# Performance work log

Hardware: AMD Instinct MI355X
Metric: run time of the kernel (lower is better)

Reference implementation:

```python
import jax, jax.numpy as jnp
import numpy as np

B, L, D = 2, 1024, 1024
H = 16
NL = 2
DFF = 4 * D
EPS = 1e-5
W_SCALE = 0.02


def rmsnorm(x, w):
    # x * rsqrt(mean(x^2, -1) + eps) * w   (computed in fp32 as in the torch code)
    xf = x.astype(jnp.float32)
    n = xf * jax.lax.rsqrt(jnp.mean(xf * xf, axis=-1, keepdims=True) + EPS)
    return n.astype(x.dtype) * w


def setup_inputs() -> dict:
    key = jax.random.key(0)
    ks = jax.random.split(key, 10)
    x = jax.random.normal(ks[0], (B, L, D), dtype=jnp.float32)
    # torch nn.Linear weight layout: [out_features, in_features]; y = x @ W.T + b
    qw = jax.random.normal(ks[1], (NL, D, D), dtype=jnp.float32) * W_SCALE
    kw = jax.random.normal(ks[2], (NL, D, D), dtype=jnp.float32) * W_SCALE
    vw = jax.random.normal(ks[3], (NL, D, D), dtype=jnp.float32) * W_SCALE
    ow = jax.random.normal(ks[4], (NL, D, D), dtype=jnp.float32) * W_SCALE
    pn_w = jnp.ones((NL, D), dtype=jnp.float32)
    ln_w = jnp.ones((NL, D), dtype=jnp.float32)
    fc_w = jax.random.normal(ks[5], (NL, DFF, D), dtype=jnp.float32) * W_SCALE
    fc2_w = jax.random.normal(ks[6], (NL, D, DFF), dtype=jnp.float32) * W_SCALE
    fc2_b = jnp.zeros((NL, D), dtype=jnp.float32)
    return {"x": x, "qw": qw, "kw": kw, "vw": vw, "ow": ow,
            "pn_w": pn_w, "ln_w": ln_w, "fc_w": fc_w, "fc2_w": fc2_w, "fc2_b": fc2_b}


def reference(x, qw, kw, vw, ow, pn_w, ln_w, fc_w, fc2_w, fc2_b):
    d = D // H
    for i in range(NL):
        # --- LinearAttention block (dropout=0 -> identity) ---
        h = rmsnorm(x, pn_w[i])                                   # [B,L,D]
        Q = (h @ qw[i].T).reshape(B, L, H, d)
        K = (h @ kw[i].T).reshape(B, L, H, d)
        V = (h @ vw[i].T).reshape(B, L, H, d)
        # outer-product state per position, cumulated over L (causal linear attn)
        W = jnp.einsum('blhd,blhe->blhde', K, V)                  # [B,L,H,d,d]
        W = jnp.cumsum(W, axis=1)
        a = jnp.einsum('blhd,blhde->blhe', Q, W).reshape(B, L, D)
        x = x + a @ ow[i].T
        # --- MLP block ---
        m = rmsnorm(x, ln_w[i])
        f = jax.nn.gelu(m @ fc_w[i].T, approximate=False)         # torch nn.GELU default = exact
        x = x + f @ fc2_w[i].T + fc2_b[i]
    return x
```

## Files before the change

kernel.cpp:

```cpp
#include <hip/hip_runtime.h>

#define BB 2
#define LL 1024
#define DD 1024
#define HH 16
#define HD 64
#define DFFN 4096
#define MM (BB*LL)
#define QS 3072

using u16 = unsigned short;
typedef __bf16 bf16x8 __attribute__((ext_vector_type(8)));
typedef float f32x4 __attribute__((ext_vector_type(4)));

__device__ __forceinline__ float b2f(u16 u) {
  union { unsigned int i; float f; } v; v.i = ((unsigned int)u) << 16; return v.f;
}
__device__ __forceinline__ u16 f2b(float f) {
  union { float f; unsigned int i; } v; v.f = f;
  unsigned int x = v.i;
  return (u16)((x + 0x7fffu + ((x >> 16) & 1u)) >> 16);
}
__device__ __forceinline__ float gelu_exact(float x) {
  return 0.5f * x * (1.0f + erff(x * 0.70710678118654752f));
}
__device__ __forceinline__ void gl2lds16(const void* g, void* l) {
  __builtin_amdgcn_global_load_lds((const __attribute__((address_space(1))) void*)g,
                                   (__attribute__((address_space(3))) void*)l, 16, 0, 0);
}

template<int N>
__device__ __forceinline__ void s_wait_vm() {
  if constexpr (N == 0)       asm volatile("s_waitcnt vmcnt(0) lgkmcnt(0)" ::: "memory");
  else if constexpr (N == 4)  asm volatile("s_waitcnt vmcnt(4) lgkmcnt(0)" ::: "memory");
  else if constexpr (N == 6)  asm volatile("s_waitcnt vmcnt(6) lgkmcnt(0)" ::: "memory");
  else if constexpr (N == 8)  asm volatile("s_waitcnt vmcnt(8) lgkmcnt(0)" ::: "memory");
  else if constexpr (N == 12) asm volatile("s_waitcnt vmcnt(12) lgkmcnt(0)" ::: "memory");
  __builtin_amdgcn_sched_barrier(0);
}

__device__ __forceinline__ void xcd_remap(int& bx, int& by, int& bz) {
  const int gx = gridDim.x, gy = gridDim.y;
  const int nb = gx * gy * gridDim.z;
  int b = blockIdx.x + gx * (blockIdx.y + gy * blockIdx.z);
  if ((nb & 127) == 0) {
    const int xcd = b & 7, seq = b >> 3;
    b = (((seq >> 4) << 3) + xcd) * 16 + (seq & 15);
  }
  bx = b % gx; const int rest = b / gx;
  by = rest % gy; bz = rest / gy;
}

__global__ __launch_bounds__(256) void castw_kernel(const float* __restrict__ in,
                                                    u16* __restrict__ out, int n8) {
  int i = blockIdx.x * 256 + threadIdx.x;
  if (i >= n8) return;
  const float4 a = reinterpret_cast<const float4*>(in)[2 * i];
  const float4 b = reinterpret_cast<const float4*>(in)[2 * i + 1];
  uint4 o;
  o.x = (unsigned)f2b(a.x) | ((unsigned)f2b(a.y) << 16);
  o.y = (unsigned)f2b(a.z) | ((unsigned)f2b(a.w) << 16);
  o.z = (unsigned)f2b(b.x) | ((unsigned)f2b(b.y) << 16);
  o.w = (unsigned)f2b(b.z) | ((unsigned)f2b(b.w) << 16);
  reinterpret_cast<uint4*>(out)[i] = o;
}
__global__ __launch_bounds__(256) void castw3_kernel(const float* __restrict__ s0,
                                                     const float* __restrict__ s1,
                                                     const float* __restrict__ s2,
                                                     u16* __restrict__ out, int n8) {
  int i = blockIdx.x * 256 + threadIdx.x;
  if (i >= n8) return;
  const float* in = (blockIdx.y == 0) ? s0 : (blockIdx.y == 1) ? s1 : s2;
  u16* dst = out + (size_t)blockIdx.y * n8 * 8;
  const float4 a = reinterpret_cast<const float4*>(in)[2 * i];
  const float4 b = reinterpret_cast<const float4*>(in)[2 * i + 1];
  uint4 o;
  o.x = (unsigned)f2b(a.x) | ((unsigned)f2b(a.y) << 16);
  o.y = (unsigned)f2b(a.z) | ((unsigned)f2b(a.w) << 16);
  o.z = (unsigned)f2b(b.x) | ((unsigned)f2b(b.y) << 16);
  o.w = (unsigned)f2b(b.z) | ((unsigned)f2b(b.w) << 16);
  reinterpret_cast<uint4*>(dst)[i] = o;
}

__global__ __launch_bounds__(256) void init_out_kernel(float* __restrict__ out,
                                                       const float* __restrict__ resid,
                                                       const float* __restrict__ bias) {
  const int i = blockIdx.x * 256 + threadIdx.x;
  float4 v = reinterpret_cast<const float4*>(resid)[i];
  if (bias != nullptr) {
    const float4 bv = *reinterpret_cast<const float4*>(bias + ((i * 4) & (DD - 1)));
    v.x += bv.x; v.y += bv.y; v.z += bv.z; v.w += bv.w;
  }
  reinterpret_cast<float4*>(out)[i] = v;
}

__global__ __launch_bounds__(256) void rmsnorm_kernel(const float* __restrict__ x,
                                                      const float* __restrict__ w,
                                                      u16* __restrict__ out) {
  const int row = blockIdx.x, t = threadIdx.x;
  const float4 v = reinterpret_cast<const float4*>(x + (size_t)row * DD)[t];
  float ss = v.x*v.x + v.y*v.y + v.z*v.z + v.w*v.w;
  #pragma unroll
  for (int o = 32; o > 0; o >>= 1) ss += __shfl_down(ss, o);
  __shared__ float red[4];
  if ((t & 63) == 0) red[t >> 6] = ss;
  __syncthreads();
  const float inv = rsqrtf((red[0] + red[1] + red[2] + red[3]) * (1.0f / DD) + 1e-5f);
  const float4 wv = reinterpret_cast<const float4*>(w)[t];
  ushort4 o;
  o.x = f2b(v.x * inv * wv.x);
  o.y = f2b(v.y * inv * wv.y);
  o.z = f2b(v.z * inv * wv.z);
  o.w = f2b(v.w * inv * wv.w);
  reinterpret_cast<ushort4*>(out + (size_t)row * DD)[t] = o;
}

template<int ROWS, int NT>
__device__ __forceinline__ void dma32(const u16* __restrict__ g, int r0, int K, int kt,
                                      int t, u16* lds) {
  #pragma unroll
  for (int i = 0; i < ROWS * 4 / NT; i++) {
    const int c = i * NT + t;
    gl2lds16(g + (size_t)(r0 + (c >> 2)) * K + kt + (c & 3) * 8, &lds[c * 8]);
  }
}
__device__ __forceinline__ void mfma_tile32(const u16* Asb, const u16* Bsb,
                                            int wm, int wn, int fr, int fq, f32x4 acc[4][4]) {
  bf16x8 af[4], bfv[4];
  #pragma unroll
  for (int i = 0; i < 4; i++)
    af[i] = *reinterpret_cast<const bf16x8*>(&Asb[(wm + i * 16 + fr) * 32 + fq * 8]);
  #pragma unroll
  for (int j = 0; j < 4; j++)
    bfv[j] = *reinterpret_cast<const bf16x8*>(&Bsb[(wn + j * 16 + fr) * 32 + fq * 8]);
  #pragma unroll
  for (int i = 0; i < 4; i++)
    #pragma unroll
    for (int j = 0; j < 4; j++)
      acc[i][j] = __builtin_amdgcn_mfma_f32_16x16x32_bf16(af[i], bfv[j], acc[i][j], 0, 0, 0);
}

template<int BM, int BN>
__device__ __forceinline__ void gemm_pipeline(const u16* __restrict__ A,
                                              const u16* __restrict__ Wb,
                                              int K, int k0, int nt, int m0, int n0,
                                              u16* As, u16* Bs, int t,
                                              int wm, int wn, int fr, int fq,
                                              f32x4 acc[4][4]) {
  constexpr int NT = (BM / 64) * (BN / 64) * 64;
  constexpr int L = (BM + BN) * 4 / NT;
  #pragma unroll
  for (int s = 0; s < 3; ++s) {
    dma32<BM, NT>(A, m0, K, k0 + s * 32, t, As + s * BM * 32);
    dma32<BN, NT>(Wb, n0, K, k0 + s * 32, t, Bs + s * BN * 32);
  }
  int pb = 0;
  for (int tt = 0; tt < nt; ++tt) {
    const int ahead = nt - 1 - tt;
    if (ahead >= 2)      s_wait_vm<2 * L>();
    else if (ahead == 1) s_wait_vm<L>();
    else                 s_wait_vm<0>();
    __builtin_amdgcn_s_barrier();
    __builtin_amdgcn_sched_barrier(0);
    if (tt + 3 < nt) {
      int p3 = pb + 3; if (p3 >= 4) p3 -= 4;
      dma32<BM, NT>(A, m0, K, k0 + (tt + 3) * 32, t, As + p3 * BM * 32);
      dma32<BN, NT>(Wb, n0, K, k0 + (tt + 3) * 32, t, Bs + p3 * BN * 32);
      __builtin_amdgcn_sched_barrier(0);
    }
    mfma_tile32(As + pb * BM * 32, Bs + pb * BN * 32, wm, wn, fr, fq, acc);
    pb = (pb + 1) & 3;
  }
}

template<int BM, int BN, int ACT>
__global__ __launch_bounds__((BM/64)*(BN/64)*64)
void mfma_gemm(const u16* __restrict__ A, const u16* __restrict__ Wb,
               u16* __restrict__ Cb, int N, int K) {
  constexpr int WCOLS = BN / 64;
  __shared__ u16 As[4 * BM * 32];
  __shared__ u16 Bs[4 * BN * 32];
  int bx, by, bz;
  xcd_remap(bx, by, bz);
  const int t = threadIdx.x;
  const int lane = t & 63, w = t >> 6;
  const int wm = (w / WCOLS) * 64, wn = (w % WCOLS) * 64;
  const int m0 = by * BM, n0 = bx * BN;
  const int fr = lane & 15, fq = lane >> 4;

  f32x4 acc[4][4] = {};
  gemm_pipeline<BM, BN>(A, Wb, K, 0, K / 32, m0, n0, As, Bs, t, wm, wn, fr, fq, acc);

  #pragma unroll
  for (int i = 0; i < 4; i++)
    #pragma unroll
    for (int j = 0; j < 4; j++)
      #pragma unroll
      for (int r = 0; r < 4; r++) {
        const int row = m0 + wm + i * 16 + fq * 4 + r;
        const int col = n0 + wn + j * 16 + fr;
        float val = acc[i][j][r];
        if (ACT == 1) val = gelu_exact(val);
        Cb[(size_t)row * N + col] = f2b(val);
      }
}

template<int BM, int BN, int SPLIT>
__global__ __launch_bounds__((BM/64)*(BN/64)*64)
void mfma_gemm_sk(const u16* __restrict__ A, const u16* __restrict__ Wb,
                  float* __restrict__ Co, int N, int K) {
  constexpr int WCOLS = BN / 64;
  __shared__ u16 As[4 * BM * 32];
  __shared__ u16 Bs[4 * BN * 32];
  int bx, by, bz;
  xcd_remap(bx, by, bz);
  const int t = threadIdx.x;
  const int lane = t & 63, w = t >> 6;
  const int wm = (w / WCOLS) * 64, wn = (w % WCOLS) * 64;
  const int m0 = by * BM, n0 = bx * BN;
  const int fr = lane & 15, fq = lane >> 4;
  const int Kc = K / SPLIT, k0 = bz * Kc;

  f32x4 acc[4][4] = {};
  gemm_pipeline<BM, BN>(A, Wb, K, k0, Kc / 32, m0, n0, As, Bs, t, wm, wn, fr, fq, acc);

  #pragma unroll
  for (int i = 0; i < 4; i++)
    #pragma unroll
    for (int j = 0; j < 4; j++)
      #pragma unroll
      for (int r = 0; r < 4; r++) {
        const int row = m0 + wm + i * 16 + fq * 4 + r;
        const int col = n0 + wn + j * 16 + fr;
        unsafeAtomicAdd(&Co[(size_t)row * N + col], acc[i][j][r]);
      }
}

__global__ __launch_bounds__(256) void kv_trans(const u16* __restrict__ QKV,
                                                u16* __restrict__ Kt, u16* __restrict__ Vt) {
  __shared__ u16 T[64][72];
  const int tile = blockIdx.x;
  const int h2 = blockIdx.y;
  const int b = blockIdx.z;
  const int h = h2 & 15, which = h2 >> 4;
  const int t = threadIdx.x;
  const int pos = t >> 2, d0 = (t & 3) * 16;
  const u16* src = QKV + ((size_t)(b * LL) + tile * 64 + pos) * QS + 1024 + which * 1024 + h * HD + d0;
  union { uint4 u[2]; u16 s[16]; } pk;
  pk.u[0] = reinterpret_cast<const uint4*>(src)[0];
  pk.u[1] = reinterpret_cast<const uint4*>(src)[1];
  #pragma unroll
  for (int j = 0; j < 16; j++) T[d0 + j][pos] = pk.s[j];
  __syncthreads();
  const int d = t >> 2, p0 = (t & 3) * 16;
  u16* dst = (which ? Vt : Kt) + ((size_t)(b * HH + h) * HD + d) * LL + tile * 64 + p0;
  union { uint4 u[2]; u16 s[16]; } ok;
  #pragma unroll
  for (int j = 0; j < 16; j++) ok.s[j] = T[d][p0 + j];
  reinterpret_cast<uint4*>(dst)[0] = ok.u[0];
  reinterpret_cast<uint4*>(dst)[1] = ok.u[1];
}

__global__ __launch_bounds__(256) void attn_phase1(const u16* __restrict__ QKV,
                                                   const u16* __restrict__ Kt,
                                                   const u16* __restrict__ Vt,
                                                   u16* __restrict__ Oa,
                                                   u16* __restrict__ Slt) {
  __shared__ u16 Ss[4][16][64];
  const int tile = blockIdx.x, h = blockIdx.y, b = blockIdx.z;
  const int t = threadIdx.x, lane = t & 63, w = t >> 6;
  const int fr = lane & 15, fq = lane >> 4;
  const size_t tok0 = (size_t)(b * LL + tile * 64);
  const size_t bh = (size_t)(b * HH + h);
  const u16* Qb  = QKV + tok0 * QS + h * HD;
  const u16* Kb  = Qb + 1024;
  const u16* Ktb = Kt + bh * (HD * LL) + tile * 64;
  const u16* Vtb = Vt + bh * (HD * LL) + tile * 64;

  bf16x8 aq[2], bk[4][2];
  #pragma unroll
  for (int kh = 0; kh < 2; kh++)
    aq[kh] = *reinterpret_cast<const bf16x8*>(Qb + (size_t)(16*w + fr) * QS + kh*32 + fq*8);
  #pragma unroll
  for (int n4 = 0; n4 < 4; n4++)
    #pragma unroll
    for (int kh = 0; kh < 2; kh++)
      bk[n4][kh] = *reinterpret_cast<const bf16x8*>(Kb + (size_t)(16*n4 + fr) * QS + kh*32 + fq*8);
  f32x4 sacc[4] = {};
  #pragma unroll
  for (int n4 = 0; n4 < 4; n4++) {
    sacc[n4] = __builtin_amdgcn_mfma_f32_16x16x32_bf16(aq[0], bk[n4][0], sacc[n4], 0, 0, 0);
    sacc[n4] = __builtin_amdgcn_mfma_f32_16x16x32_bf16(aq[1], bk[n4][1], sacc[n4], 0, 0, 0);
  }
  #pragma unroll
  for (int n4 = 0; n4 < 4; n4++)
    #pragma unroll
    for (int r = 0; r < 4; r++) {
      const bool keep = (16*w + 4*fq + r) >= (16*n4 + fr);
      Ss[w][4*fq + r][16*n4 + fr] = keep ? f2b(sacc[n4][r]) : (u16)0;
    }
  __syncthreads();

  bf16x8 va[2], kt[4][2];
  #pragma unroll
  for (int kh = 0; kh < 2; kh++)
    va[kh] = *reinterpret_cast<const bf16x8*>(Vtb + (size_t)(16*w + fr) * LL + kh*32 + fq*8);
  #pragma unroll
  for (int n4 = 0; n4 < 4; n4++)
    #pragma unroll
    for (int kh = 0; kh < 2; kh++)
      kt[n4][kh] = *reinterpret_cast<const bf16x8*>(Ktb + (size_t)(16*n4 + fr) * LL + kh*32 + fq*8);
  f32x4 lacc[4] = {};
  #pragma unroll
  for (int n4 = 0; n4 < 4; n4++) {
    lacc[n4] = __builtin_amdgcn_mfma_f32_16x16x32_bf16(va[0], kt[n4][0], lacc[n4], 0, 0, 0);
    lacc[n4] = __builtin_amdgcn_mfma_f32_16x16x32_bf16(va[1], kt[n4][1], lacc[n4], 0, 0, 0);
  }
  u16* So = Slt + (bh * 16 + tile) * 4096;
  #pragma unroll
  for (int n4 = 0; n4 < 4; n4++)
    #pragma unroll
    for (int r = 0; r < 4; r++)
      So[(size_t)(16*w + 4*fq + r) * 64 + 16*n4 + fr] = f2b(lacc[n4][r]);

  bf16x8 sa[2], vb[4][2];
  #pragma unroll
  for (int kh = 0; kh < 2; kh++)
    sa[kh] = *reinterpret_cast<const bf16x8*>(&Ss[w][fr][kh*32 + fq*8]);
  #pragma unroll
  for (int n4 = 0; n4 < 4; n4++)
    #pragma unroll
    for (int kh = 0; kh < 2; kh++)
      vb[n4][kh] = *reinterpret_cast<const bf16x8*>(Vtb + (size_t)(16*n4 + fr) * LL + kh*32 + fq*8);
  f32x4 oacc[4] = {};
  #pragma unroll
  for (int n4 = 0; n4 < 4; n4++) {
    oacc[n4] = __builtin_amdgcn_mfma_f32_16x16x32_bf16(sa[0], vb[n4][0], oacc[n4], 0, 0, 0);
    oacc[n4] = __builtin_amdgcn_mfma_f32_16x16x32_bf16(sa[1], vb[n4][1], oacc[n4], 0, 0, 0);
  }
  u16* Ob = Oa + (tok0 + 16*w) * DD + h * HD;
  #pragma unroll
  for (int n4 = 0; n4 < 4; n4++)
    #pragma unroll
    for (int r = 0; r < 4; r++)
      Ob[(size_t)(4*fq + r) * DD + 16*n4 + fr] = f2b(oacc[n4][r]);
}

__global__ __launch_bounds__(256) void attn_phase2(const u16* __restrict__ Slt,
                                                   u16* __restrict__ Wc) {
  const int rg = blockIdx.x, h = blockIdx.y, b = blockIdx.z;
  const size_t base = ((size_t)((b * HH + h) * 16)) * 4096 + rg * 512 + threadIdx.x * 2;
  float r0 = 0.f, r1 = 0.f;
  for (int tl = 0; tl < 16; tl++) {
    const size_t p = base + (size_t)tl * 4096;
    const unsigned d = *reinterpret_cast<const unsigned*>(Slt + p);
    *reinterpret_cast<unsigned*>(Wc + p) = (unsigned)f2b(r0) | ((unsigned)f2b(r1) << 16);
    r0 += b2f((u16)(d & 0xffff));
    r1 += b2f((u16)(d >> 16));
  }
}

__global__ __launch_bounds__(256) void attn_phase3(const u16* __restrict__ QKV,
                                                   const u16* __restrict__ Wc,
                                                   u16* __restrict__ Oa) {
  const int tile = blockIdx.x, h = blockIdx.y, b = blockIdx.z;
  const int t = threadIdx.x, lane = t & 63, w = t >> 6;
  const int fr = lane & 15, fq = lane >> 4;
  const size_t tok0 = (size_t)(b * LL + tile * 64);
  const size_t bh = (size_t)(b * HH + h);
  const u16* Qb = QKV + tok0 * QS + h * HD;
  const u16* Wb = Wc + (bh * 16 + tile) * 4096;

  bf16x8 aq[2], wb[4][2];
  #pragma unroll
  for (int kh = 0; kh < 2; kh++)
    aq[kh] = *reinterpret_cast<const bf16x8*>(Qb + (size_t)(16*w + fr) * QS + kh*32 + fq*8);
  #pragma unroll
  for (int n4 = 0; n4 < 4; n4++)
    #pragma unroll
    for (int kh = 0; kh < 2; kh++)
      wb[n4][kh] = *reinterpret_cast<const bf16x8*>(Wb + (size_t)(16*n4 + fr) * 64 + kh*32 + fq*8);
  f32x4 oacc[4] = {};
  #pragma unroll
  for (int n4 = 0; n4 < 4; n4++) {
    oacc[n4] = __builtin_amdgcn_mfma_f32_16x16x32_bf16(aq[0], wb[n4][0], oacc[n4], 0, 0, 0);
    oacc[n4] = __builtin_amdgcn_mfma_f32_16x16x32_bf16(aq[1], wb[n4][1], oacc[n4], 0, 0, 0);
  }
  u16* Ob = Oa + (tok0 + 16*w) * DD + h * HD;
  #pragma unroll
  for (int n4 = 0; n4 < 4; n4++)
    #pragma unroll
    for (int r = 0; r < 4; r++) {
      const size_t idx = (size_t)(4*fq + r) * DD + 16*n4 + fr;
      Ob[idx] = f2b(b2f(Ob[idx]) + oacc[n4][r]);
    }
}

extern "C" void kernel_launch(void* const* d_in, const int* in_sizes, int n_in,
                              void* d_out, int out_size, void* d_ws, size_t ws_size,
                              hipStream_t stream) {
  const float* x_in = (const float*)d_in[0];
  const float* qw   = (const float*)d_in[1];
  const float* kw   = (const float*)d_in[2];
  const float* vw   = (const float*)d_in[3];
  const float* ow   = (const float*)d_in[4];
  const float* pn   = (const float*)d_in[5];
  const float* ln   = (const float*)d_in[6];
  const float* fcw  = (const float*)d_in[7];
  const float* fc2w = (const float*)d_in[8];
  const float* fc2b = (const float*)d_in[9];

  char* ws = (char*)d_ws;
  u16* wbuf = (u16*)ws;
  u16* slt  = (u16*)ws;
  u16* wcum = (u16*)(ws + (size_t)(4 << 20));
  u16* h    = (u16*)(ws + (size_t)(8 << 20));
  u16* qkv  = (u16*)(ws + (size_t)(12 << 20));
  u16* f    = (u16*)(ws + (size_t)(12 << 20));
  u16* vt   = (u16*)(ws + (size_t)(24 << 20));
  u16* kt   = (u16*)(ws + (size_t)(28 << 20));
  float* xf = (float*)d_out;

  const int n8D = DD * DD / 8;
  const int n8F = DFFN * DD / 8;
  const int gInit = MM * DD / 4 / 256;

  for (int i = 0; i < 2; i++) {
    const float* qwi  = qw   + (size_t)i * DD * DD;
    const float* kwi  = kw   + (size_t)i * DD * DD;
    const float* vwi  = vw   + (size_t)i * DD * DD;
    const float* owi  = ow   + (size_t)i * DD * DD;
    const float* fcwi = fcw  + (size_t)i * DFFN * DD;
    const float* f2wi = fc2w + (size_t)i * DD * DFFN;
    const float* src  = (i == 0) ? x_in : xf;

    rmsnorm_kernel<<<MM, 256, 0, stream>>>(src, pn + i * DD, h);
    castw3_kernel<<<dim3(n8D / 256, 3), 256, 0, stream>>>(qwi, kwi, vwi, wbuf, n8D);
    mfma_gemm<128, 64, 0><<<dim3(QS / 64, MM / 128), 128, 0, stream>>>(
        h, wbuf, qkv, QS, DD);
    kv_trans<<<dim3(16, 32, BB), 256, 0, stream>>>(qkv, kt, vt);
    attn_phase1<<<dim3(16, HH, BB), 256, 0, stream>>>(qkv, kt, vt, h, slt);
    attn_phase2<<<dim3(8, HH, BB), 256, 0, stream>>>(slt, wcum);
    attn_phase3<<<dim3(16, HH, BB), 256, 0, stream>>>(qkv, wcum, h);
    castw_kernel<<<n8D / 256, 256, 0, stream>>>(owi, wbuf, n8D);
    init_out_kernel<<<gInit, 256, 0, stream>>>(xf, src, nullptr);
    mfma_gemm_sk<128, 64, 2><<<dim3(DD / 64, MM / 128, 2), 128, 0, stream>>>(
        h, wbuf, xf, DD, DD);
    rmsnorm_kernel<<<MM, 256, 0, stream>>>(xf, ln + i * DD, h);
    castw_kernel<<<n8F / 256, 256, 0, stream>>>(fcwi, wbuf, n8F);
    mfma_gemm<128, 64, 1><<<dim3(DFFN / 64, MM / 128), 128, 0, stream>>>(
        h, wbuf, f, DFFN, DD);
    castw_kernel<<<n8F / 256, 256, 0, stream>>>(f2wi, wbuf, n8F);
    float* co = (i == 1) ? (float*)d_out : xf;
    init_out_kernel<<<gInit, 256, 0, stream>>>(co, xf, fc2b + i * DD);
    mfma_gemm_sk<128, 64, 4><<<dim3(DD / 64, MM / 128, 4), 128, 0, stream>>>(
        f, wbuf, co, DD, DFFN);
  }
}
```

Before: 583.5 us.

## Replace 4-stage GEMM pipeline with single-buffer BK=64 swizzled loop, raise split-K

Drops the 4-deep multi-buffered global-to-LDS pipeline with explicit vmcnt waits. In its place is a simple synchronous loop that loads 64-wide K tiles into one swizzled LDS buffer and does two MFMA k-steps per tile. The LDS layout interleaves rows and k-chunks to cut bank conflicts, and split-K factors for the output-projection and FC2 GEMMs are doubled for more parallelism. The trade is losing load/compute overlap for fewer barriers, lower LDS use and higher occupancy, while adding more atomic traffic.

After: 678.5 us. 16.3% more time.

```diff
diff --git a/kernel.cpp b/kernel.cpp
--- a/kernel.cpp
+++ b/kernel.cpp
@@ -27,16 +27,6 @@
 __device__ __forceinline__ void gl2lds16(const void* g, void* l) {
   __builtin_amdgcn_global_load_lds((const __attribute__((address_space(1))) void*)g,
                                    (__attribute__((address_space(3))) void*)l, 16, 0, 0);
-}
-
-template<int N>
-__device__ __forceinline__ void s_wait_vm() {
-  if constexpr (N == 0)       asm volatile("s_waitcnt vmcnt(0) lgkmcnt(0)" ::: "memory");
-  else if constexpr (N == 4)  asm volatile("s_waitcnt vmcnt(4) lgkmcnt(0)" ::: "memory");
-  else if constexpr (N == 6)  asm volatile("s_waitcnt vmcnt(6) lgkmcnt(0)" ::: "memory");
-  else if constexpr (N == 8)  asm volatile("s_waitcnt vmcnt(8) lgkmcnt(0)" ::: "memory");
-  else if constexpr (N == 12) asm volatile("s_waitcnt vmcnt(12) lgkmcnt(0)" ::: "memory");
-  __builtin_amdgcn_sched_barrier(0);
 }
 
 __device__ __forceinline__ void xcd_remap(int& bx, int& by, int& bz) {
@@ -116,60 +106,55 @@
 }
 
 template<int ROWS, int NT>
-__device__ __forceinline__ void dma32(const u16* __restrict__ g, int r0, int K, int kt,
+__device__ __forceinline__ void dma64(const u16* __restrict__ g, int r0, int K, int kt,
                                       int t, u16* lds) {
   #pragma unroll
-  for (int i = 0; i < ROWS * 4 / NT; i++) {
+  for (int i = 0; i < ROWS * 8 / NT; i++) {
     const int c = i * NT + t;
-    gl2lds16(g + (size_t)(r0 + (c >> 2)) * K + kt + (c & 3) * 8, &lds[c * 8]);
-  }
-}
-__device__ __forceinline__ void mfma_tile32(const u16* Asb, const u16* Bsb,
+    const int row = (c & 7) | ((c >> 6) << 3);
+    const int kc = (c >> 3) & 7;
+    gl2lds16(g + (size_t)(r0 + row) * K + kt + kc * 8, &lds[c * 8]);
+  }
+}
+__device__ __forceinline__ const bf16x8* lds_frag64(const u16* base, int r, int q) {
+  const int p = (r & 7) | (q << 3) | ((r >> 3) << 6);
+  return reinterpret_cast<const bf16x8*>(&base[p * 8]);
+}
+
+#define MFMA_BF16 __builtin_amdgcn_mfma_f32_16x16x32_bf16
+
+__device__ __forceinline__ void mfma_tile64(const u16* Asb, const u16* Bsb,
                                             int wm, int wn, int fr, int fq, f32x4 acc[4][4]) {
-  bf16x8 af[4], bfv[4];
-  #pragma unroll
-  for (int i = 0; i < 4; i++)
-    af[i] = *reinterpret_cast<const bf16x8*>(&Asb[(wm + i * 16 + fr) * 32 + fq * 8]);
-  #pragma unroll
-  for (int j = 0; j < 4; j++)
-    bfv[j] = *reinterpret_cast<const bf16x8*>(&Bsb[(wn + j * 16 + fr) * 32 + fq * 8]);
-  #pragma unroll
-  for (int i = 0; i < 4; i++)
-    #pragma unroll
-    for (int j = 0; j < 4; j++)
-      acc[i][j] = __builtin_amdgcn_mfma_f32_16x16x32_bf16(af[i], bfv[j], acc[i][j], 0, 0, 0);
+  #pragma unroll
+  for (int kk = 0; kk < 2; kk++) {
+    const int q = kk * 4 + fq;
+    bf16x8 af[4], bfv[4];
+    #pragma unroll
+    for (int i = 0; i < 4; i++) af[i] = *lds_frag64(Asb, wm + i * 16 + fr, q);
+    #pragma unroll
+    for (int j = 0; j < 4; j++) bfv[j] = *lds_frag64(Bsb, wn + j * 16 + fr, q);
+    #pragma unroll
+    for (int i = 0; i < 4; i++)
+      #pragma unroll
+      for (int j = 0; j < 4; j++)
+        acc[i][j] = MFMA_BF16(af[i], bfv[j], acc[i][j], 0, 0, 0);
+  }
 }
 
 template<int BM, int BN>
-__device__ __forceinline__ void gemm_pipeline(const u16* __restrict__ A,
-                                              const u16* __restrict__ Wb,
-                                              int K, int k0, int nt, int m0, int n0,
-                                              u16* As, u16* Bs, int t,
-                                              int wm, int wn, int fr, int fq,
-                                              f32x4 acc[4][4]) {
+__device__ __forceinline__ void gemm_loop(const u16* __restrict__ A,
+                                          const u16* __restrict__ Wb,
+                                          int K, int k0, int kend, int m0, int n0,
+                                          u16* As, u16* Bs, int t,
+                                          int wm, int wn, int fr, int fq,
+                                          f32x4 acc[4][4]) {
   constexpr int NT = (BM / 64) * (BN / 64) * 64;
-  constexpr int L = (BM + BN) * 4 / NT;
-  #pragma unroll
-  for (int s = 0; s < 3; ++s) {
-    dma32<BM, NT>(A, m0, K, k0 + s * 32, t, As + s * BM * 32);
-    dma32<BN, NT>(Wb, n0, K, k0 + s * 32, t, Bs + s * BN * 32);
-  }
-  int pb = 0;
-  for (int tt = 0; tt < nt; ++tt) {
-    const int ahead = nt - 1 - tt;
-    if (ahead >= 2)      s_wait_vm<2 * L>();
-    else if (ahead == 1) s_wait_vm<L>();
-    else                 s_wait_vm<0>();
-    __builtin_amdgcn_s_barrier();
-    __builtin_amdgcn_sched_barrier(0);
-    if (tt + 3 < nt) {
-      int p3 = pb + 3; if (p3 >= 4) p3 -= 4;
-      dma32<BM, NT>(A, m0, K, k0 + (tt + 3) * 32, t, As + p3 * BM * 32);
-      dma32<BN, NT>(Wb, n0, K, k0 + (tt + 3) * 32, t, Bs + p3 * BN * 32);
-      __builtin_amdgcn_sched_barrier(0);
-    }
-    mfma_tile32(As + pb * BM * 32, Bs + pb * BN * 32, wm, wn, fr, fq, acc);
-    pb = (pb + 1) & 3;
+  for (int kt = k0; kt < kend; kt += 64) {
+    dma64<BM, NT>(A, m0, K, kt, t, As);
+    dma64<BN, NT>(Wb, n0, K, kt, t, Bs);
+    __syncthreads();
+    mfma_tile64(As, Bs, wm, wn, fr, fq, acc);
+    __syncthreads();
   }
 }
 
@@ -178,8 +163,8 @@
 void mfma_gemm(const u16* __restrict__ A, const u16* __restrict__ Wb,
                u16* __restrict__ Cb, int N, int K) {
   constexpr int WCOLS = BN / 64;
-  __shared__ u16 As[4 * BM * 32];
-  __shared__ u16 Bs[4 * BN * 32];
+  __shared__ u16 As[BM * 64];
+  __shared__ u16 Bs[BN * 64];
   int bx, by, bz;
   xcd_remap(bx, by, bz);
   const int t = threadIdx.x;
@@ -189,7 +174,7 @@
   const int fr = lane & 15, fq = lane >> 4;
 
   f32x4 acc[4][4] = {};
-  gemm_pipeline<BM, BN>(A, Wb, K, 0, K / 32, m0, n0, As, Bs, t, wm, wn, fr, fq, acc);
+  gemm_loop<BM, BN>(A, Wb, K, 0, K, m0, n0, As, Bs, t, wm, wn, fr, fq, acc);
 
   #pragma unroll
   for (int i = 0; i < 4; i++)
@@ -210,8 +195,8 @@
 void mfma_gemm_sk(const u16* __restrict__ A, const u16* __restrict__ Wb,
                   float* __restrict__ Co, int N, int K) {
   constexpr int WCOLS = BN / 64;
-  __shared__ u16 As[4 * BM * 32];
-  __shared__ u16 Bs[4 * BN * 32];
+  __shared__ u16 As[BM * 64];
+  __shared__ u16 Bs[BN * 64];
   int bx, by, bz;
   xcd_remap(bx, by, bz);
   const int t = threadIdx.x;
@@ -222,7 +207,7 @@
   const int Kc = K / SPLIT, k0 = bz * Kc;
 
   f32x4 acc[4][4] = {};
-  gemm_pipeline<BM, BN>(A, Wb, K, k0, Kc / 32, m0, n0, As, Bs, t, wm, wn, fr, fq, acc);
+  gemm_loop<BM, BN>(A, Wb, K, k0, k0 + Kc, m0, n0, As, Bs, t, wm, wn, fr, fq, acc);
 
   #pragma unroll
   for (int i = 0; i < 4; i++)
@@ -289,8 +274,8 @@
   f32x4 sacc[4] = {};
   #pragma unroll
   for (int n4 = 0; n4 < 4; n4++) {
-    sacc[n4] = __builtin_amdgcn_mfma_f32_16x16x32_bf16(aq[0], bk[n4][0], sacc[n4], 0, 0, 0);
-    sacc[n4] = __builtin_amdgcn_mfma_f32_16x16x32_bf16(aq[1], bk[n4][1], sacc[n4], 0, 0, 0);
+    sacc[n4] = MFMA_BF16(aq[0], bk[n4][0], sacc[n4], 0, 0, 0);
+    sacc[n4] = MFMA_BF16(aq[1], bk[n4][1], sacc[n4], 0, 0, 0);
   }
   #pragma unroll
   for (int n4 = 0; n4 < 4; n4++)
@@ -313,8 +298,8 @@
   f32x4 lacc[4] = {};
   #pragma unroll
   for (int n4 = 0; n4 < 4; n4++) {
-    lacc[n4] = __builtin_amdgcn_mfma_f32_16x16x32_bf16(va[0], kt[n4][0], lacc[n4], 0, 0, 0);
-    lacc[n4] = __builtin_amdgcn_mfma_f32_16x16x32_bf16(va[1], kt[n4][1], lacc[n4], 0, 0, 0);
+    lacc[n4] = MFMA_BF16(va[0], kt[n4][0], lacc[n4], 0, 0, 0);
+    lacc[n4] = MFMA_BF16(va[1], kt[n4][1], lacc[n4], 0, 0, 0);
   }
   u16* So = Slt + (bh * 16 + tile) * 4096;
   #pragma unroll
@@ -335,8 +320,8 @@
   f32x4 oacc[4] = {};
   #pragma unroll
   for (int n4 = 0; n4 < 4; n4++) {
-    oacc[n4] = __builtin_amdgcn_mfma_f32_16x16x32_bf16(sa[0], vb[n4][0], oacc[n4], 0, 0, 0);
-    oacc[n4] = __builtin_amdgcn_mfma_f32_16x16x32_bf16(sa[1], vb[n4][1], oacc[n4], 0, 0, 0);
+    oacc[n4] = MFMA_BF16(sa[0], vb[n4][0], oacc[n4], 0, 0, 0);
+    oacc[n4] = MFMA_BF16(sa[1], vb[n4][1], oacc[n4], 0, 0, 0);
   }
   u16* Ob = Oa + (tok0 + 16*w) * DD + h * HD;
   #pragma unroll
@@ -383,8 +368,8 @@
   f32x4 oacc[4] = {};
   #pragma unroll
   for (int n4 = 0; n4 < 4; n4++) {
-    oacc[n4] = __builtin_amdgcn_mfma_f32_16x16x32_bf16(aq[0], wb[n4][0], oacc[n4], 0, 0, 0);
-    oacc[n4] = __builtin_amdgcn_mfma_f32_16x16x32_bf16(aq[1], wb[n4][1], oacc[n4], 0, 0, 0);
+    oacc[n4] = MFMA_BF16(aq[0], wb[n4][0], oacc[n4], 0, 0, 0);
+    oacc[n4] = MFMA_BF16(aq[1], wb[n4][1], oacc[n4], 0, 0, 0);
   }
   u16* Ob = Oa + (tok0 + 16*w) * DD + h * HD;
   #pragma unroll
@@ -444,7 +429,7 @@
     attn_phase3<<<dim3(16, HH, BB), 256, 0, stream>>>(qkv, wcum, h);
     castw_kernel<<<n8D / 256, 256, 0, stream>>>(owi, wbuf, n8D);
     init_out_kernel<<<gInit, 256, 0, stream>>>(xf, src, nullptr);
-    mfma_gemm_sk<128, 64, 2><<<dim3(DD / 64, MM / 128, 2), 128, 0, stream>>>(
+    mfma_gemm_sk<128, 64, 4><<<dim3(DD / 64, MM / 128, 4), 128, 0, stream>>>(
         h, wbuf, xf, DD, DD);
     rmsnorm_kernel<<<MM, 256, 0, stream>>>(xf, ln + i * DD, h);
     castw_kernel<<<n8F / 256, 256, 0, stream>>>(fcwi, wbuf, n8F);
@@ -453,7 +438,7 @@
     castw_kernel<<<n8F / 256, 256, 0, stream>>>(f2wi, wbuf, n8F);
     float* co = (i == 1) ? (float*)d_out : xf;
     init_out_kernel<<<gInit, 256, 0, stream>>>(co, xf, fc2b + i * DD);
-    mfma_gemm_sk<128, 64, 4><<<dim3(DD / 64, MM / 128, 4), 128, 0, stream>>>(
+    mfma_gemm_sk<128, 64, 8><<<dim3(DD / 64, MM / 128, 8), 128, 0, stream>>>(
         f, wbuf, co, DD, DFFN);
   }
 }
```
